# Kernel tuning notes

Hardware: AMD Instinct MI355X
Metric: run time of the kernel (lower is better)

The kernel has to match this reference:

```python
import jax, jax.numpy as jnp
import numpy as np

DIM = 512
CODEBOOK_SIZE = 2048
NUM_Q = 8
COMMIT_W = 0.25
B, T = 8, 2048


def setup_inputs() -> dict:
    key = jax.random.key(0)
    k1, k2 = jax.random.split(key)
    x = jax.random.normal(k1, (B, T, DIM), dtype=jnp.float32)
    lim = 1.0 / CODEBOOK_SIZE
    codebooks = jax.random.uniform(k2, (NUM_Q, CODEBOOK_SIZE, DIM), dtype=jnp.float32,
                                   minval=-lim, maxval=lim)
    return {"x": x, "codebooks": codebooks}


def reference(x, codebooks):
    """Residual VQ forward.
    x: (B, T, D); codebooks: (Q, K, D).
    Returns (quantized (B,T,D), indices (B,T,Q) int32, mean loss scalar).
    """
    sg = jax.lax.stop_gradient
    residual = x
    quantized = jnp.zeros_like(x)
    idx_list = []
    total_loss = jnp.zeros((), dtype=x.dtype)
    for i in range(NUM_Q):
        cb = codebooks[i]  # (K, D)
        # squared L2 distances: (B,T,K)
        d = (jnp.sum(residual * residual, axis=-1, keepdims=True)
             - 2.0 * jnp.einsum('btd,kd->btk', residual, cb)
             + jnp.sum(cb * cb, axis=-1))
        min_idx = jnp.argmin(d, axis=-1)  # (B,T)
        idx_list.append(min_idx)
        q_lvl = cb[min_idx]  # (B,T,D) gather
        quantized = quantized + q_lvl
        commit_loss = jnp.mean((sg(residual) - q_lvl) ** 2)
        codebook_loss = jnp.mean((residual - sg(q_lvl)) ** 2)
        total_loss = total_loss + commit_loss * COMMIT_W + codebook_loss
        residual = residual - sg(q_lvl)
    # straight-through estimator
    quantized = x + sg(quantized - x)
    indices = jnp.stack(idx_list, axis=-1)  # (B,T,Q)
    return quantized, indices, total_loss / NUM_Q
```

## Files before the change

### kernel.cpp

```cpp
#include <hip/hip_runtime.h>


constexpr int DIM   = 512;
constexpr int KCB   = 2048;
constexpr int NQ    = 8;
constexpr int NTOK  = 8 * 2048;
constexpr int QELEM = NTOK * DIM;
constexpr int NBLK  = KCB / 128;
constexpr float WINDOW = 1e-3f;

using short8  = __attribute__((ext_vector_type(8))) short;
using float4v = __attribute__((ext_vector_type(4))) float;

__device__ __forceinline__ unsigned short f2bf(float f) {
    unsigned u = __float_as_uint(f);
    return (unsigned short)((u + 0x7FFFu + ((u >> 16) & 1u)) >> 16);
}

__device__ __forceinline__ void gl2lds16(const void* g, void* l) {
    __builtin_amdgcn_global_load_lds(
        (__attribute__((address_space(1))) void*)g,
        (__attribute__((address_space(3))) void*)l, 16, 0, 0);
}

struct Top4 { float s[4]; int i[4]; };
__device__ __forceinline__ void t4_init(Top4& t) {
#pragma unroll
    for (int j = 0; j < 4; ++j) { t.s[j] = 3.0e38f; t.i[j] = 0x7FFFFFFF; }
}
__device__ __forceinline__ void t4_ins(Top4& t, float s, int idx) {
    if (s < t.s[3]) {
        if (s < t.s[2]) { t.s[3] = t.s[2]; t.i[3] = t.i[2];
            if (s < t.s[1]) { t.s[2] = t.s[1]; t.i[2] = t.i[1];
                if (s < t.s[0]) { t.s[1] = t.s[0]; t.i[1] = t.i[0]; t.s[0] = s; t.i[0] = idx; }
                else            { t.s[1] = s; t.i[1] = idx; }
            } else { t.s[2] = s; t.i[2] = idx; }
        } else { t.s[3] = s; t.i[3] = idx; }
    }
}

__global__ __launch_bounds__(256) void k_initnorm(
        const float* __restrict__ x, const float* __restrict__ cbs,
        float4* __restrict__ R, ushort4* __restrict__ Rb, ushort4* __restrict__ Cbb,
        float* __restrict__ r2, float* __restrict__ c2)
{
#pragma clang fp contract(off)
    __shared__ float buf[4][DIM];
    __shared__ float accs[4][32];
    const int w = threadIdx.x >> 6, lane = threadIdx.x & 63;
    const bool isX = blockIdx.x < (NTOK / 4);
    const int row = (isX ? blockIdx.x : blockIdx.x - NTOK / 4) * 4 + w;

    const float* src = isX ? x : cbs;
    const float4* a4 = reinterpret_cast<const float4*>(src + (size_t)row * DIM);
    float4 v0 = a4[lane], v1 = a4[lane + 64];

    ushort4 b0 = make_ushort4(f2bf(v0.x), f2bf(v0.y), f2bf(v0.z), f2bf(v0.w));
    ushort4 b1 = make_ushort4(f2bf(v1.x), f2bf(v1.y), f2bf(v1.z), f2bf(v1.w));
    if (isX) {
        R [(size_t)row * 128 + lane]      = v0;
        R [(size_t)row * 128 + lane + 64] = v1;
        Rb[(size_t)row * 128 + lane]      = b0;
        Rb[(size_t)row * 128 + lane + 64] = b1;
    } else {
        Cbb[(size_t)row * 128 + lane]      = b0;
        Cbb[(size_t)row * 128 + lane + 64] = b1;
    }

    float4* b4 = reinterpret_cast<float4*>(buf[w]);
    b4[lane]      = v0;
    b4[lane + 64] = v1;
    __syncthreads();
    if (lane < 32) {
        int blk = lane >> 3, j = lane & 7;
        const float* p = buf[w] + blk * 128 + j;
        float x0 = p[0];
        float acc = x0 * x0;
#pragma unroll
        for (int m = 1; m < 16; ++m) { float xx = p[8 * m]; acc = acc + xx * xx; }
        accs[w][lane] = acc;
    }
    __syncthreads();
    if (lane == 0) {
        float B[4];
#pragma unroll
        for (int blk = 0; blk < 4; ++blk) {
            const float* r = &accs[w][blk * 8];
            B[blk] = ((r[0] + r[1]) + (r[2] + r[3])) + ((r[4] + r[5]) + (r[6] + r[7]));
        }
        float out = (B[0] + B[1]) + (B[2] + B[3]);
        if (isX) r2[row] = out; else c2[row] = out;
    }
}

__global__ __launch_bounds__(256, 3) void k_gemm_topk(
        const unsigned short* __restrict__ Rb, const unsigned short* __restrict__ Cbb,
        const float* __restrict__ c2, float* __restrict__ candS, int* __restrict__ candI)
{
    __shared__ __align__(16) char smem[49664];
    unsigned short* A0 = (unsigned short*)smem;
    unsigned short* B0 = (unsigned short*)(smem + 24576);
    float*  scb = (float*)smem;
    float*  c2s = (float*)(smem + 49152);

    const int tid  = threadIdx.x;
    const int wid  = tid >> 6, lane = tid & 63;
    const int quad = lane >> 4, l16 = lane & 15;

    const int L    = blockIdx.y * NBLK + blockIdx.x;
    const int slot = L >> 3;
    const int mb   = (L & 7) * 16 + (slot >> 4);
    const int nb   = slot & 15;

    const int tok0 = mb * 128, n0 = nb * 128;
    const int nw = (wid & 1) * 64;
    const int fbA = (wid >> 1) * 4;
    const int fbB = (wid & 1) * 4;

    if (tid < 128) c2s[tid] = c2[n0 + tid];

    float4v acc[4][4];
    float4v zero = {0.f, 0.f, 0.f, 0.f};
#pragma unroll
    for (int mi = 0; mi < 4; ++mi)
#pragma unroll
        for (int nj = 0; nj < 4; ++nj) acc[mi][nj] = zero;

    auto stage = [&](int b, int kb) {
        unsigned short* Ad = A0 + b * 4096;
        unsigned short* Bd = B0 + b * 4096;
#pragma unroll
        for (int i = 0; i < 2; ++i) {
            int mi_abs = i * 4 + wid;
            gl2lds16(&Rb[(size_t)(tok0 + mi_abs * 16 + l16) * DIM + kb + quad * 8],
                     Ad + (size_t)(i * 256 + wid * 64) * 8);
            gl2lds16(&Cbb[(size_t)(n0 + mi_abs * 16 + l16) * DIM + kb + quad * 8],
                     Bd + (size_t)(i * 256 + wid * 64) * 8);
        }
    };

    auto compute = [&](int b) {
        const unsigned short* Ac = A0 + b * 4096;
        const unsigned short* Bc = B0 + b * 4096;
        short8 af[4], bf[4];
#pragma unroll
        for (int mi = 0; mi < 4; ++mi)
            af[mi] = *(const short8*)(Ac + ((size_t)(fbA + mi) * 64 + lane) * 8);
#pragma unroll
        for (int nj = 0; nj < 4; ++nj)
            bf[nj] = *(const short8*)(Bc + ((size_t)(fbB + nj) * 64 + lane) * 8);
        __builtin_amdgcn_s_setprio(1);
#pragma unroll
        for (int mi = 0; mi < 4; ++mi)
#pragma unroll
            for (int nj = 0; nj < 4; ++nj)
                acc[mi][nj] = __builtin_amdgcn_mfma_f32_16x16x32_bf16(
                    af[mi], bf[nj], acc[mi][nj], 0, 0, 0);
        __builtin_amdgcn_s_setprio(0);
    };

    stage(0, 0);
    stage(1, 32);
    int cur = 0, pf = 2;
    for (int it = 0; it < 15; ++it) {
        asm volatile("s_waitcnt vmcnt(4)" ::: "memory");
        __builtin_amdgcn_s_barrier();
        __builtin_amdgcn_sched_barrier(0);
        if (it < 14) stage(pf, (it + 2) * 32);
        compute(cur);
        cur = (cur == 2) ? 0 : cur + 1;
        pf  = (pf  == 2) ? 0 : pf  + 1;
    }
    asm volatile("s_waitcnt vmcnt(0)" ::: "memory");
    __builtin_amdgcn_s_barrier();
    __builtin_amdgcn_sched_barrier(0);
    compute(cur);

    const int row_ = tid >> 2, part_ = tid & 3;
    float4 c2r[8];
#pragma unroll
    for (int j = 0; j < 8; ++j)
        c2r[j] = *(const float4*)(c2s + part_ * 32 + 4 * j);

    for (int h = 0; h < 2; ++h) {
        __syncthreads();
        if ((wid >> 1) == h) {
#pragma unroll
            for (int mi = 0; mi < 4; ++mi)
#pragma unroll
                for (int nj = 0; nj < 4; ++nj) {
                    int r0 = mi * 16 + quad * 4;
                    int cc = nw + nj * 16 + l16;
#pragma unroll
                    for (int e = 0; e < 4; ++e)
                        scb[(r0 + e) * 132 + cc] = acc[mi][nj][e];
                }
        }
        __syncthreads();
        Top4 t; t4_init(t);
#pragma unroll
        for (int j = 0; j < 8; ++j) {
            float4 sv = *(const float4*)(scb + row_ * 132 + part_ * 32 + 4 * j);
            float4 cv = c2r[j];
            int c0 = n0 + part_ * 32 + 4 * j;
            t4_ins(t, cv.x - 2.0f * sv.x, c0 + 0);
            t4_ins(t, cv.y - 2.0f * sv.y, c0 + 1);
            t4_ins(t, cv.z - 2.0f * sv.z, c0 + 2);
            t4_ins(t, cv.w - 2.0f * sv.w, c0 + 3);
        }
#pragma unroll
        for (int k = 1; k <= 2; k <<= 1) {
            float os[4]; int oi[4];
#pragma unroll
            for (int j = 0; j < 4; ++j) {
                os[j] = __shfl_xor(t.s[j], k, 64);
                oi[j] = __shfl_xor(t.i[j], k, 64);
            }
#pragma unroll
            for (int j = 0; j < 4; ++j) t4_ins(t, os[j], oi[j]);
        }
        if (part_ == 0) {
            int token = tok0 + h * 64 + row_;
            size_t base = (size_t)token * 64 + (size_t)nb * 4;
#pragma unroll
            for (int j = 0; j < 4; ++j) { candS[base + j] = t.s[j]; candI[base + j] = t.i[j]; }
        }
    }
}

__global__ __launch_bounds__(256) void k_selupd(
        const float* __restrict__ candS, const int* __restrict__ candI,
        float* __restrict__ R, const float* __restrict__ cbf,
        float* __restrict__ r2, const float* __restrict__ c2,
        float* __restrict__ idx_out, float* __restrict__ partial,
        ushort4* __restrict__ Rb, const float4* __restrict__ x, int level)
{
#pragma clang fp contract(off)
    __shared__ float buf[4][DIM];
    __shared__ float accs[4][32];
    __shared__ float shl[4];
    const int w = threadIdx.x >> 6, lane = threadIdx.x & 63;
    const int t = blockIdx.x * 4 + w;
    const bool last = (level == NQ - 1);

    float4* r4 = reinterpret_cast<float4*>(R + (size_t)t * DIM);
    float4* b4 = reinterpret_cast<float4*>(buf[w]);
    float4 rr[2];
    rr[0] = r4[lane];      rr[1] = r4[lane + 64];
    b4[lane] = rr[0];      b4[lane + 64] = rr[1];

    float sb = candS[(size_t)t * 64 + lane];
    int   ci = candI[(size_t)t * 64 + lane];
    float mn = sb;
#pragma unroll
    for (int off = 32; off; off >>= 1) mn = fminf(mn, __shfl_xor(mn, off, 64));
    unsigned long long mask = __ballot(sb <= mn + WINDOW);
    int ncand = __popcll(mask);
    int winner;
    if (ncand == 1) {
        winner = __shfl(ci, __ffsll(mask) - 1, 64);
    } else {
        int src = 0;
        if (lane < ncand) {
            unsigned long long mm = mask;
            for (int z = 0; z < lane; ++z) mm &= mm - 1;
            src = __ffsll(mm) - 1;
        }
        int cidx = __shfl(ci, src, 64);
        float s = 3.0e38f;
        int   si = 0x7FFFFFFF;
        if (lane < ncand) {
            const float4* cp4 = reinterpret_cast<const float4*>(cbf + (size_t)cidx * DIM);
            const float4* rp4 = reinterpret_cast<const float4*>(buf[w]);
            float d = 0.f;
#pragma unroll 4
            for (int j = 0; j < DIM / 4; ++j) {
                float4 cv = cp4[j];
                float4 rv = rp4[j];
                d = fmaf(rv.x, cv.x, d);
                d = fmaf(rv.y, cv.y, d);
                d = fmaf(rv.z, cv.z, d);
                d = fmaf(rv.w, cv.w, d);
            }
            float td = 2.0f * d;
            float a  = r2[t] - td;
            s  = a + c2[cidx];
            si = cidx;
        }
#pragma unroll
        for (int off = 32; off; off >>= 1) {
            float ov = __shfl_xor(s, off, 64);
            int   oi = __shfl_xor(si, off, 64);
            if (ov < s || (ov == s && oi < si)) { s = ov; si = oi; }
        }
        winner = si;
    }
    if (lane == 0) idx_out[(size_t)t * NQ + level] = (float)winner;

    const float4* c4 = reinterpret_cast<const float4*>(cbf + (size_t)winner * DIM);
    float ls = 0.f;
#pragma unroll
    for (int i = 0; i < 2; ++i) {
        int d = lane + 64 * i;
        float4 rv = rr[i], cv = c4[d];
        rv.x -= cv.x; rv.y -= cv.y; rv.z -= cv.z; rv.w -= cv.w;
        ls = ls + rv.x * rv.x; ls = ls + rv.y * rv.y;
        ls = ls + rv.z * rv.z; ls = ls + rv.w * rv.w;
        if (!last) {
            r4[d] = rv;
            b4[d] = rv;
            Rb[(size_t)t * 128 + d] = make_ushort4(f2bf(rv.x), f2bf(rv.y),
                                                   f2bf(rv.z), f2bf(rv.w));
        } else {
            float4 xv = x[(size_t)t * 128 + d];
            xv.x -= rv.x; xv.y -= rv.y; xv.z -= rv.z; xv.w -= rv.w;
            r4[d] = xv;
        }
    }

    if (!last) {
        __syncthreads();
        if (lane < 32) {
            int blk = lane >> 3, j = lane & 7;
            const float* p = buf[w] + blk * 128 + j;
            float x0 = p[0];
            float acc = x0 * x0;
#pragma unroll
            for (int m = 1; m < 16; ++m) { float xx = p[8 * m]; acc = acc + xx * xx; }
            accs[w][lane] = acc;
        }
        __syncthreads();
        if (lane == 0) {
            float B[4];
#pragma unroll
            for (int blk = 0; blk < 4; ++blk) {
                const float* r = &accs[w][blk * 8];
                B[blk] = ((r[0] + r[1]) + (r[2] + r[3])) + ((r[4] + r[5]) + (r[6] + r[7]));
            }
            r2[t] = (B[0] + B[1]) + (B[2] + B[3]);
        }
    }

#pragma unroll
    for (int off = 32; off; off >>= 1) ls += __shfl_down(ls, off, 64);
    if (lane == 0) shl[w] = ls;
    __syncthreads();
    if (threadIdx.x == 0) partial[blockIdx.x] = (shl[0] + shl[1]) + (shl[2] + shl[3]);
}

__global__ __launch_bounds__(256) void k_finalize_loss(const float* __restrict__ partial,
                                                       float* __restrict__ loss_out)
{
    double s = 0.0;
    for (int i = threadIdx.x; i < NQ * (NTOK / 4); i += 256) s += (double)partial[i];
#pragma unroll
    for (int off = 32; off; off >>= 1) s += __shfl_down(s, off, 64);
    __shared__ double sh[4];
    if ((threadIdx.x & 63) == 0) sh[threadIdx.x >> 6] = s;
    __syncthreads();
    if (threadIdx.x == 0) {
        double tot = (sh[0] + sh[1]) + (sh[2] + sh[3]);
        loss_out[0] = (float)(tot * 1.25 / ((double)NQ * (double)QELEM));
    }
}

extern "C" void kernel_launch(void* const* d_in, const int* in_sizes, int n_in,
                              void* d_out, int out_size, void* d_ws, size_t ws_size,
                              hipStream_t stream)
{
    const float* x   = (const float*)d_in[0];
    const float* cbs = (const float*)d_in[1];

    float* qout     = (float*)d_out;
    float* idx_out  = qout + QELEM;
    float* loss_out = idx_out + (size_t)NTOK * NQ;
    float* R        = qout;

    char* ws = (char*)d_ws;
    size_t off = 0;
    unsigned short* Rb   = (unsigned short*)(ws + off); off += (size_t)QELEM * 2;
    unsigned short* Cbb  = (unsigned short*)(ws + off); off += (size_t)QELEM * 2;
    float*          c2   = (float*)(ws + off);          off += (size_t)NQ * KCB * 4;
    float*          r2   = (float*)(ws + off);          off += (size_t)NTOK * 4;
    float*          part = (float*)(ws + off);          off += (size_t)NQ * (NTOK / 4) * 4;
    float*          candS= (float*)(ws + off);          off += (size_t)NTOK * 64 * 4;
    int*            candI= (int*)(ws + off);            off += (size_t)NTOK * 64 * 4;

    k_initnorm<<<NTOK / 4 + NQ * KCB / 4, 256, 0, stream>>>(
        x, cbs, (float4*)R, (ushort4*)Rb, (ushort4*)Cbb, r2, c2);

    for (int q = 0; q < NQ; ++q) {
        const float*          cbq  = cbs + (size_t)q * KCB * DIM;
        const unsigned short* cbbq = Cbb + (size_t)q * KCB * DIM;
        const float*          c2q  = c2 + (size_t)q * KCB;
        dim3 g(NBLK, NTOK / 128);
        k_gemm_topk<<<g, 256, 0, stream>>>(Rb, cbbq, c2q, candS, candI);
        k_selupd<<<NTOK / 4, 256, 0, stream>>>(candS, candI, R, cbq, r2, c2q,
                                               idx_out, part + (size_t)q * (NTOK / 4),
                                               (ushort4*)Rb, (const float4*)x, q);
    }

    k_finalize_loss<<<1, 256, 0, stream>>>(part, loss_out);
}
```

Baseline: 1.006 ms.

## Enlarge GEMM+top-k block tile to 256x256 with 512 threads

Increases the distance GEMM block tile from 128x128 to 256x256 with 8 waves, each computing a 128x64 sub-tile of 8x4 MFMA fragments. The larger tile halves global/L2 traffic per output and improves operand reuse from LDS. The top-k epilogue is reorganized into four 64-row passes over a wider scratch buffer, and candidate slots still map to 128-column groups. In exchange it uses about 97KB of LDS and more accumulator registers per block, which reduces occupancy and halves the grid size.

```diff
diff --git a/kernel.cpp b/kernel.cpp
--- a/kernel.cpp
+++ b/kernel.cpp
@@ -6,7 +6,7 @@
 constexpr int NQ    = 8;
 constexpr int NTOK  = 8 * 2048;
 constexpr int QELEM = NTOK * DIM;
-constexpr int NBLK  = KCB / 128;
+constexpr int NBLK2 = KCB / 256;
 constexpr float WINDOW = 1e-3f;
 
 using short8  = __attribute__((ext_vector_type(8))) short;
@@ -93,65 +93,67 @@
     }
 }
 
-__global__ __launch_bounds__(256, 3) void k_gemm_topk(
+__global__ __launch_bounds__(512, 2) void k_gemm_topk(
         const unsigned short* __restrict__ Rb, const unsigned short* __restrict__ Cbb,
         const float* __restrict__ c2, float* __restrict__ candS, int* __restrict__ candI)
 {
-    __shared__ __align__(16) char smem[49664];
-    unsigned short* A0 = (unsigned short*)smem;
-    unsigned short* B0 = (unsigned short*)(smem + 24576);
+    __shared__ __align__(16) char smem[99328];
+    unsigned short* As = (unsigned short*)smem;
+    unsigned short* Bs = (unsigned short*)(smem + 49152);
     float*  scb = (float*)smem;
-    float*  c2s = (float*)(smem + 49152);
+    float*  c2s = (float*)(smem + 98304);
 
     const int tid  = threadIdx.x;
     const int wid  = tid >> 6, lane = tid & 63;
     const int quad = lane >> 4, l16 = lane & 15;
-
-    const int L    = blockIdx.y * NBLK + blockIdx.x;
+    const int wr = wid >> 2, wc = wid & 3;
+
+    const int L    = blockIdx.y * NBLK2 + blockIdx.x;
     const int slot = L >> 3;
-    const int mb   = (L & 7) * 16 + (slot >> 4);
-    const int nb   = slot & 15;
-
-    const int tok0 = mb * 128, n0 = nb * 128;
-    const int nw = (wid & 1) * 64;
-    const int fbA = (wid >> 1) * 4;
-    const int fbB = (wid & 1) * 4;
-
-    if (tid < 128) c2s[tid] = c2[n0 + tid];
-
-    float4v acc[4][4];
+    const int mb   = (L & 7) * 8 + (slot >> 3);
+    const int nb2  = slot & 7;
+
+    const int tok0 = mb * 256, n0 = nb2 * 256;
+
+    if (tid < 256) c2s[tid] = c2[n0 + tid];
+
+    float4v acc[8][4];
     float4v zero = {0.f, 0.f, 0.f, 0.f};
 #pragma unroll
-    for (int mi = 0; mi < 4; ++mi)
+    for (int mi = 0; mi < 8; ++mi)
 #pragma unroll
         for (int nj = 0; nj < 4; ++nj) acc[mi][nj] = zero;
 
-    auto stage = [&](int b, int kb) {
-        unsigned short* Ad = A0 + b * 4096;
-        unsigned short* Bd = B0 + b * 4096;
-#pragma unroll
-        for (int i = 0; i < 2; ++i) {
-            int mi_abs = i * 4 + wid;
-            gl2lds16(&Rb[(size_t)(tok0 + mi_abs * 16 + l16) * DIM + kb + quad * 8],
-                     Ad + (size_t)(i * 256 + wid * 64) * 8);
-            gl2lds16(&Cbb[(size_t)(n0 + mi_abs * 16 + l16) * DIM + kb + quad * 8],
-                     Bd + (size_t)(i * 256 + wid * 64) * 8);
+    auto stage = [&](int b3, int kb) {
+        unsigned short* Ad = As + b3 * 8192;
+        unsigned short* Bd = Bs + b3 * 8192;
+#pragma unroll
+        for (int c = 0; c < 2; ++c) {
+            int g = wid * 2 + c;
+            gl2lds16(&Rb[(size_t)(tok0 + g * 16 + l16) * DIM + kb + quad * 8],
+                     Ad + (size_t)(g * 64) * 8);
+        }
+#pragma unroll
+        for (int c = 0; c < 2; ++c) {
+            int g = wid * 2 + c;
+            gl2lds16(&Cbb[(size_t)(n0 + g * 16 + l16) * DIM + kb + quad * 8],
+                     Bd + (size_t)(g * 64) * 8);
         }
     };
 
-    auto compute = [&](int b) {
-        const unsigned short* Ac = A0 + b * 4096;
-        const unsigned short* Bc = B0 + b * 4096;
-        short8 af[4], bf[4];
-#pragma unroll
-        for (int mi = 0; mi < 4; ++mi)
-            af[mi] = *(const short8*)(Ac + ((size_t)(fbA + mi) * 64 + lane) * 8);
+    auto compute = [&](int b3) {
+        const unsigned short* Ac = As + b3 * 8192;
+        const unsigned short* Bc = Bs + b3 * 8192;
+        short8 af[8], bf[4];
+#pragma unroll
+        for (int mi = 0; mi < 8; ++mi)
+            af[mi] = *(const short8*)(Ac + ((size_t)(wr * 8 + mi) * 64 + lane) * 8);
 #pragma unroll
         for (int nj = 0; nj < 4; ++nj)
-            bf[nj] = *(const short8*)(Bc + ((size_t)(fbB + nj) * 64 + lane) * 8);
+            bf[nj] = *(const short8*)(Bc + ((size_t)(wc * 4 + nj) * 64 + lane) * 8);
         __builtin_amdgcn_s_setprio(1);
 #pragma unroll
-        for (int mi = 0; mi < 4; ++mi)
+        for (int mi = 0; mi < 8; ++mi)
 #pragma unroll
             for (int nj = 0; nj < 4; ++nj)
                 acc[mi][nj] = __builtin_amdgcn_mfma_f32_16x16x32_bf16(
@@ -161,48 +163,44 @@
 
     stage(0, 0);
     stage(1, 32);
-    int cur = 0, pf = 2;
-    for (int it = 0; it < 15; ++it) {
-        asm volatile("s_waitcnt vmcnt(4)" ::: "memory");
+    for (int it = 0; it < 16; ++it) {
+        if (it < 15) asm volatile("s_waitcnt vmcnt(4)" ::: "memory");
+        else         asm volatile("s_waitcnt vmcnt(0)" ::: "memory");
         __builtin_amdgcn_s_barrier();
         __builtin_amdgcn_sched_barrier(0);
-        if (it < 14) stage(pf, (it + 2) * 32);
-        compute(cur);
-        cur = (cur == 2) ? 0 : cur + 1;
-        pf  = (pf  == 2) ? 0 : pf  + 1;
-    }
-    asm volatile("s_waitcnt vmcnt(0)" ::: "memory");
-    __builtin_amdgcn_s_barrier();
-    __builtin_amdgcn_sched_barrier(0);
-    compute(cur);
-
-    const int row_ = tid >> 2, part_ = tid & 3;
+        if (it < 14) stage((it + 2) % 3, (it + 2) * 32);
+        compute(it % 3);
+    }
+
+    const int row_ = tid >> 3, pp = tid & 7;
     float4 c2r[8];
 #pragma unroll
     for (int j = 0; j < 8; ++j)
-        c2r[j] = *(const float4*)(c2s + part_ * 32 + 4 * j);
-
-    for (int h = 0; h < 2; ++h) {
+        c2r[j] = *(const float4*)(c2s + pp * 32 + 4 * j);
+
+#pragma unroll
+    for (int qr = 0; qr < 4; ++qr) {
         __syncthreads();
-        if ((wid >> 1) == h) {
-#pragma unroll
-            for (int mi = 0; mi < 4; ++mi)
+        if (wr == (qr >> 1)) {
+            const int mi0 = (qr & 1) * 4;
+#pragma unroll
+            for (int mm = 0; mm < 4; ++mm)
 #pragma unroll
                 for (int nj = 0; nj < 4; ++nj) {
-                    int r0 = mi * 16 + quad * 4;
-                    int cc = nw + nj * 16 + l16;
+                    int r0 = mm * 16 + quad * 4;
+                    int cc = wc * 64 + nj * 16 + l16;
 #pragma unroll
                     for (int e = 0; e < 4; ++e)
-                        scb[(r0 + e) * 132 + cc] = acc[mi][nj][e];
+                        scb[(r0 + e) * 260 + cc] = acc[mi0 + mm][nj][e];
                 }
         }
         __syncthreads();
         Top4 t; t4_init(t);
 #pragma unroll
         for (int j = 0; j < 8; ++j) {
-            float4 sv = *(const float4*)(scb + row_ * 132 + part_ * 32 + 4 * j);
+            float4 sv = *(const float4*)(scb + row_ * 260 + pp * 32 + 4 * j);
             float4 cv = c2r[j];
-            int c0 = n0 + part_ * 32 + 4 * j;
+            int c0 = n0 + pp * 32 + 4 * j;
             t4_ins(t, cv.x - 2.0f * sv.x, c0 + 0);
             t4_ins(t, cv.y - 2.0f * sv.y, c0 + 1);
             t4_ins(t, cv.z - 2.0f * sv.z, c0 + 2);
@@ -219,8 +217,9 @@
 #pragma unroll
             for (int j = 0; j < 4; ++j) t4_ins(t, os[j], oi[j]);
         }
-        if (part_ == 0) {
-            int token = tok0 + h * 64 + row_;
+        if ((pp & 3) == 0) {
+            int token = tok0 + qr * 64 + row_;
+            int nb = nb2 * 2 + (pp >> 2);
             size_t base = (size_t)token * 64 + (size_t)nb * 4;
 #pragma unroll
             for (int j = 0; j < 4; ++j) { candS[base + j] = t.s[j]; candI[base + j] = t.i[j]; }
@@ -393,8 +392,8 @@
         const float*          cbq  = cbs + (size_t)q * KCB * DIM;
         const unsigned short* cbbq = Cbb + (size_t)q * KCB * DIM;
         const float*          c2q  = c2 + (size_t)q * KCB;
-        dim3 g(NBLK, NTOK / 128);
-        k_gemm_topk<<<g, 256, 0, stream>>>(Rb, cbbq, c2q, candS, candI);
+        dim3 g(NBLK2, NTOK / 256);
+        k_gemm_topk<<<g, 512, 0, stream>>>(Rb, cbbq, c2q, candS, candI);
         k_selupd<<<NTOK / 4, 256, 0, stream>>>(candS, candI, R, cbq, r2, c2q,
                                                idx_out, part + (size_t)q * (NTOK / 4),
                                                (ushort4*)Rb, (const float4*)x, q);
```

Result: no change. 992.6 us (-1.3%).

## Switch GEMM to double buffering for higher occupancy and split top-4 chains

Applied to the files above, without the earlier changes.

Shrinks the GEMM-topk kernel's LDS footprint from a triple-buffered to a double-buffered A/B pipeline and raises launch bounds from 3 to 4 blocks per CU to gain occupancy. The main loop now uses a plain __syncthreads with one prefetch stage ahead instead of vmcnt-tuned waits. The top-4 selection is split into four independent partial lists merged at the end, shortening the serial dependency chain. Trade-offs are less latency hiding per block, tighter register limits that may spill, and extra merge work.

```diff
diff --git a/kernel.cpp b/kernel.cpp
--- a/kernel.cpp
+++ b/kernel.cpp
@@ -93,15 +93,15 @@
     }
 }
 
-__global__ __launch_bounds__(256, 3) void k_gemm_topk(
+__global__ __launch_bounds__(256, 4) void k_gemm_topk(
         const unsigned short* __restrict__ Rb, const unsigned short* __restrict__ Cbb,
         const float* __restrict__ c2, float* __restrict__ candS, int* __restrict__ candI)
 {
-    __shared__ __align__(16) char smem[49664];
+    __shared__ __align__(16) char smem[34304];
     unsigned short* A0 = (unsigned short*)smem;
-    unsigned short* B0 = (unsigned short*)(smem + 24576);
+    unsigned short* B0 = (unsigned short*)(smem + 16384);
     float*  scb = (float*)smem;
-    float*  c2s = (float*)(smem + 49152);
+    float*  c2s = (float*)(smem + 33792);
 
     const int tid  = threadIdx.x;
     const int wid  = tid >> 6, lane = tid & 63;
@@ -160,21 +160,11 @@
     };
 
     stage(0, 0);
-    stage(1, 32);
-    int cur = 0, pf = 2;
-    for (int it = 0; it < 15; ++it) {
-        asm volatile("s_waitcnt vmcnt(4)" ::: "memory");
-        __builtin_amdgcn_s_barrier();
-        __builtin_amdgcn_sched_barrier(0);
-        if (it < 14) stage(pf, (it + 2) * 32);
-        compute(cur);
-        cur = (cur == 2) ? 0 : cur + 1;
-        pf  = (pf  == 2) ? 0 : pf  + 1;
-    }
-    asm volatile("s_waitcnt vmcnt(0)" ::: "memory");
-    __builtin_amdgcn_s_barrier();
-    __builtin_amdgcn_sched_barrier(0);
-    compute(cur);
+    for (int it = 0; it < 16; ++it) {
+        __syncthreads();
+        if (it < 15) stage((it + 1) & 1, (it + 1) * 32);
+        compute(it & 1);
+    }
 
     const int row_ = tid >> 2, part_ = tid & 3;
     float4 c2r[8];
@@ -197,17 +187,28 @@
                 }
         }
         __syncthreads();
-        Top4 t; t4_init(t);
-#pragma unroll
-        for (int j = 0; j < 8; ++j) {
-            float4 sv = *(const float4*)(scb + row_ * 132 + part_ * 32 + 4 * j);
-            float4 cv = c2r[j];
-            int c0 = n0 + part_ * 32 + 4 * j;
-            t4_ins(t, cv.x - 2.0f * sv.x, c0 + 0);
-            t4_ins(t, cv.y - 2.0f * sv.y, c0 + 1);
-            t4_ins(t, cv.z - 2.0f * sv.z, c0 + 2);
-            t4_ins(t, cv.w - 2.0f * sv.w, c0 + 3);
-        }
+        Top4 tc[4];
+#pragma unroll
+        for (int c = 0; c < 4; ++c) t4_init(tc[c]);
+#pragma unroll
+        for (int c = 0; c < 4; ++c) {
+#pragma unroll
+            for (int v = 0; v < 2; ++v) {
+                int j = c * 2 + v;
+                float4 sv = *(const float4*)(scb + row_ * 132 + part_ * 32 + 4 * j);
+                float4 cv = c2r[j];
+                int c0 = n0 + part_ * 32 + 4 * j;
+                t4_ins(tc[c], cv.x - 2.0f * sv.x, c0 + 0);
+                t4_ins(tc[c], cv.y - 2.0f * sv.y, c0 + 1);
+                t4_ins(tc[c], cv.z - 2.0f * sv.z, c0 + 2);
+                t4_ins(tc[c], cv.w - 2.0f * sv.w, c0 + 3);
+            }
+        }
+#pragma unroll
+        for (int c = 1; c < 4; ++c)
+#pragma unroll
+            for (int j = 0; j < 4; ++j) t4_ins(tc[0], tc[c].s[j], tc[c].i[j]);
+        Top4 t = tc[0];
 #pragma unroll
         for (int k = 1; k <= 2; k <<= 1) {
             float os[4]; int oi[4];
```

New measurement: 1.284 ms. 1.28x slower.
